# Optimization experiments

Hardware: AMD Instinct MI355X
Metric: run time of the kernel (lower is better)

## Reference

```python
import jax, jax.numpy as jnp
import numpy as np

ROPE_BASE = 100.0  # croco/dust3r RoPE2D default freq


def _rope1d(tok, pos1d, base=ROPE_BASE):
    # tok: [B,H,N,D], pos1d: [B,N] int
    D = tok.shape[-1]
    half = D // 2
    inv_freq = 1.0 / (base ** (jnp.arange(0, D, 2, dtype=jnp.float32) / D))  # [D/2]
    ang = pos1d[..., None].astype(jnp.float32) * inv_freq                    # [B,N,D/2]
    ang = jnp.concatenate([ang, ang], axis=-1)                               # [B,N,D]
    cos = jnp.cos(ang)[:, None, :, :].astype(tok.dtype)  # [B,1,N,D]
    sin = jnp.sin(ang)[:, None, :, :].astype(tok.dtype)
    t1, t2 = tok[..., :half], tok[..., half:]
    rot = jnp.concatenate([-t2, t1], axis=-1)  # rotate_half
    return tok * cos + rot * sin


def rope2d(tok, pos, base=ROPE_BASE):
    # tok: [B,H,N,C], pos: [B,N,2] (y,x) integer coords
    D = tok.shape[-1] // 2
    y = _rope1d(tok[..., :D], pos[..., 0], base)
    x = _rope1d(tok[..., D:], pos[..., 1], base)
    return jnp.concatenate([y, x], axis=-1)


def setup_inputs() -> dict:
    key = jax.random.key(0)
    k1, k2, k3, k4, k5 = jax.random.split(key, 5)
    B, H, N, C = 2, 12, 2049, 64
    q = jax.random.normal(k1, (B, H, N, C), dtype=jnp.float32)
    k = jax.random.normal(k2, (B, H, N, C), dtype=jnp.float32)
    v = jax.random.normal(k3, (B, H, N, C), dtype=jnp.float32)
    qpos = jax.random.randint(k4, (B, N, 2), 0, 64, dtype=jnp.int32)
    kpos = jax.random.randint(k5, (B, N, 2), 0, 64, dtype=jnp.int32)
    mask_for_attention = jnp.ones((B, N, N), dtype=bool)
    return {"q": q, "k": k, "v": v, "qpos": qpos, "kpos": kpos,
            "mask_for_attention": mask_for_attention, "num_cls": 1}


def reference(q, k, v, qpos, kpos, mask_for_attention, num_cls):
    B, H, Nq, C = q.shape
    scale = C ** -0.5
    # split off cls tokens, apply RoPE only to positional tokens
    q_nc = rope2d(q[:, :, num_cls:], qpos[:, num_cls:])
    k_nc = rope2d(k[:, :, num_cls:], kpos[:, num_cls:])
    # block similarity matrix:
    #            | K_cls |   K_pos    |
    #   | Q_cls |        sim_qcls_k   |
    #   |       | sim_q |-------------|
    #   | Q_pos |        |  sim_rope  |
    sim_rope = jnp.einsum('bhqc,bhkc->bhqk', q_nc, k_nc)                      # [B,H,Nq-cls,Nk-cls]
    sim_qcls_k = jnp.einsum('bhqc,bhkc->bhqk', q[:, :, :num_cls], k[:, :, num_cls:])
    sim_q = jnp.einsum('bhqc,bhkc->bhqk', q, k[:, :, :num_cls])               # [B,H,Nq,cls]
    sim = jnp.concatenate([sim_qcls_k, sim_rope], axis=-2)
    sim = jnp.concatenate([sim_q, sim], axis=-1)                              # [B,H,Nq,Nk]
    sim = sim * scale
    sim = jnp.where(mask_for_attention[:, None], sim, -jnp.inf)
    attn = jax.nn.softmax(sim, axis=-1)
    x = jnp.einsum('bhqk,bhkc->bhqc', attn, v)
    return x.transpose(0, 2, 1, 3).reshape(B, Nq, C * H)
```

## Files before the change

### kernel.cpp

```cpp
#include <hip/hip_runtime.h>
#include <hip/hip_bf16.h>

typedef __attribute__((ext_vector_type(8))) short bf16x8;
typedef __attribute__((ext_vector_type(4))) float f32x4;
typedef __attribute__((ext_vector_type(2))) float f32x2;
typedef unsigned short u16;

#define BN 2
#define HN 12
#define NN 2049
#define CN 64
#define NT 2048
#define BH 24
#define SCALE 0.125f
#define QSCL 0.1803368801111204f

__device__ __forceinline__ u16 f2bf(float x) {
  unsigned u = __builtin_bit_cast(unsigned, x);
  unsigned r = (u + 0x7fffu + ((u >> 16) & 1u)) >> 16;
  return (u16)r;
}

__device__ __forceinline__ unsigned cvt_pk(float lo, float hi) {
  unsigned r;
  asm("v_cvt_pk_bf16_f32 %0, %1, %2" : "=v"(r) : "v"(lo), "v"(hi));
  return r;
}

union PU {
  unsigned u[4];
  bf16x8 v;
};

__global__ __launch_bounds__(256) void rope_pack(
    const float* __restrict__ q, const float* __restrict__ k, const float* __restrict__ v,
    const int* __restrict__ qpos, const int* __restrict__ kpos,
    u16* __restrict__ Qr, u16* __restrict__ Kr, u16* __restrict__ Vt,
    float* __restrict__ S0, float* __restrict__ Pl, float* __restrict__ Po) {
  const int bh = blockIdx.x;
  const int t = blockIdx.y;
  const int b = bh / HN;
  const int tid = threadIdx.x;
  const int wv = tid >> 6, l = tid & 63;

  __shared__ float lutc[1024], luts[1024];
  __shared__ float qs[4096], ks[4096];
  __shared__ u16 ldsV[64][72];
  __shared__ float q0s[64], k0s[64];
  __shared__ float osum[4][64];
  __shared__ float psum[4];

  const int n0 = 1 + t * 64;
  const size_t base0 = (size_t)bh * NN * CN;

  const float LF = 6.6438561897747253f / 16.0f;
  for (int i = tid; i < 1024; i += 256) {
    const int pos = i >> 4, f = i & 15;
    const float inv = exp2f(-(float)f * LF);
    float sv, cv;
    sincosf((float)pos * inv, &sv, &cv);
    lutc[i] = cv;
    luts[i] = sv;
  }
  if (tid < 64) {
    q0s[tid] = q[base0 + tid];
    k0s[tid] = k[base0 + tid];
  }
  for (int e = tid; e < 4096; e += 256) {
    const int tok = e >> 6, c = e & 63;
    const size_t base = base0 + (size_t)(n0 + tok) * CN;
    qs[e] = q[base + c];
    ks[e] = k[base + c];
  }
  __syncthreads();

  float oacc = 0.f, pacc = 0.f;
  for (int i = 0; i < 16; ++i) {
    const int tok = i * 4 + wv;
    const int c = l;
    const int n = n0 + tok;
    const int cp = c & 31, f = cp & 15, axis = c >> 5;
    const int qp_ = qpos[((size_t)b * NN + n) * 2 + axis];
    const int kp_ = kpos[((size_t)b * NN + n) * 2 + axis];
    const float qa = qs[tok * 64 + c];
    const float ka = ks[tok * 64 + c];
    const float qrot = (cp < 16) ? -qs[tok * 64 + c + 16] : qs[tok * 64 + c - 16];
    const float krot = (cp < 16) ? -ks[tok * 64 + c + 16] : ks[tok * 64 + c - 16];
    Qr[((size_t)bh * NT + (n - 1)) * CN + c] =
        f2bf((qa * lutc[qp_ * 16 + f] + qrot * luts[qp_ * 16 + f]) * QSCL);
    Kr[((size_t)bh * NT + (n - 1)) * CN + c] =
        f2bf(ka * lutc[kp_ * 16 + f] + krot * luts[kp_ * 16 + f]);
    const float vv = v[base0 + (size_t)n * CN + c];
    ldsV[c][tok] = f2bf(vv);

    float pk = ka * q0s[c];
    float pq = qa * k0s[c];
    pk += __shfl_xor(pk, 1, 64);  pq += __shfl_xor(pq, 1, 64);
    pk += __shfl_xor(pk, 2, 64);  pq += __shfl_xor(pq, 2, 64);
    pk += __shfl_xor(pk, 4, 64);  pq += __shfl_xor(pq, 4, 64);
    pk += __shfl_xor(pk, 8, 64);  pq += __shfl_xor(pq, 8, 64);
    pk += __shfl_xor(pk, 16, 64); pq += __shfl_xor(pq, 16, 64);
    pk += __shfl_xor(pk, 32, 64); pq += __shfl_xor(pq, 32, 64);
    const float p = __builtin_amdgcn_exp2f(pk * QSCL);
    pacc += p;
    oacc += p * vv;
    if (l == 0) S0[(size_t)bh * NT + (n - 1)] = pq * QSCL;
  }
  osum[wv][l] = oacc;
  if (l == 0) psum[wv] = pacc;
  __syncthreads();

  for (int e = tid; e < 4096; e += 256) {
    const int c = e >> 6, tok = e & 63;
    Vt[((size_t)bh * CN + c) * NT + (t * 64 + tok)] = ldsV[c][tok];
  }
  if (tid < 64)
    Po[(size_t)(bh * 32 + t) * 64 + tid] =
        osum[0][tid] + osum[1][tid] + osum[2][tid] + osum[3][tid];
  if (tid == 0) Pl[bh * 32 + t] = psum[0] + psum[1] + psum[2] + psum[3];
}

__global__ __launch_bounds__(64) void row0_reduce(
    const float* __restrict__ q, const float* __restrict__ k, const float* __restrict__ v,
    const float* __restrict__ Pl, const float* __restrict__ Po, float* __restrict__ out) {
  const int bh = blockIdx.x;
  const int b = bh / HN, h = bh % HN;
  const int c = threadIdx.x;
  const size_t base0 = (size_t)bh * NN * CN;
  float pr = q[base0 + c] * k[base0 + c];
  pr += __shfl_xor(pr, 1, 64);
  pr += __shfl_xor(pr, 2, 64);
  pr += __shfl_xor(pr, 4, 64);
  pr += __shfl_xor(pr, 8, 64);
  pr += __shfl_xor(pr, 16, 64);
  pr += __shfl_xor(pr, 32, 64);
  const float p00 = __builtin_amdgcn_exp2f(pr * QSCL);
  float L = p00;
  float acc = p00 * v[base0 + c];
#pragma unroll
  for (int i = 0; i < 32; ++i) {
    L += Pl[bh * 32 + i];
    acc += Po[(size_t)(bh * 32 + i) * 64 + c];
  }
  out[(size_t)b * NN * (HN * CN) + h * CN + c] = acc / L;
}

__global__ __launch_bounds__(256) void attn_main(
    const float* __restrict__ v,
    const u16* __restrict__ Qr, const u16* __restrict__ Kr, const u16* __restrict__ Vt,
    const float* __restrict__ S0, float* __restrict__ out) {
  const int wg = blockIdx.x;
  const int bh = wg >> 5, qt = wg & 31;
  const int b = bh / HN, h = bh % HN;
  const int tid = threadIdx.x;
  const int wv = tid >> 6, l = tid & 63;
  const int l15 = l & 15, l4 = l >> 4;

  __shared__ u16 ldsK[2][4096];
  __shared__ u16 ldsV[2][4096];
  __shared__ float v0f[64];

  if (tid < 64) v0f[tid] = v[(size_t)bh * NN * CN + tid];
  __syncthreads();

  const int qrow = qt * 64 + wv * 16 + l15;
  const u16* qp = Qr + ((size_t)bh * NT + qrow) * CN;
  const bf16x8 qf0 = *reinterpret_cast<const bf16x8*>(qp + l4 * 8);
  const bf16x8 qf1 = *reinterpret_cast<const bf16x8*>(qp + 32 + l4 * 8);

  const float s0l2 = S0[(size_t)bh * NT + qrow];

  float lsum = (l4 == 0) ? __builtin_amdgcn_exp2f(s0l2) : 0.f;
  f32x4 o[4];
#pragma unroll
  for (int r = 0; r < 4; ++r) {
    const float p0 = __builtin_amdgcn_exp2f(__shfl(s0l2, (l4 << 2) | r, 64));
#pragma unroll
    for (int cf = 0; cf < 4; ++cf) o[cf][r] = p0 * v0f[cf * 16 + l15];
  }

  const u16* Kbh = Kr + (size_t)bh * NT * CN;
  const u16* Vbh = Vt + (size_t)bh * CN * NT;
  char* ldsKc = reinterpret_cast<char*>(&ldsK[0][0]);
  char* ldsVc = reinterpret_cast<char*>(&ldsV[0][0]);

  const int s16 = tid & 7, srowA = tid >> 3, srowB = (tid >> 3) + 32;
  const int swzA = (srowA & 7) << 4, swzB = (srowB & 7) << 4;
  const int kofsA = srowA * 128 + ((s16 * 16) ^ swzA);
  const int kofsB = srowB * 128 + ((s16 * 16) ^ swzB);
  const int pA = 2 * (32 * (s16 >> 2) + 8 * ((2 * s16) & 3) + 4 * ((s16 >> 1) & 1));
  const int pB = 2 * (32 * (s16 >> 2) + 8 * ((2 * s16 + 1) & 3) + 4 * ((s16 >> 1) & 1));
  const int vofsA0 = srowA * 128 + (pA ^ swzA);
  const int vofsA1 = srowA * 128 + (pB ^ swzA);
  const int vofsB0 = srowB * 128 + (pA ^ swzB);
  const int vofsB1 = srowB * 128 + (pB ^ swzB);

  f32x4 kreg[2], vrg[2];
#define LOAD_TILE(nx)                                                                       \
  do {                                                                                      \
    kreg[0] = *reinterpret_cast<const f32x4*>(Kbh + (size_t)((nx) + srowA) * CN + s16 * 8); \
    kreg[1] = *reinterpret_cast<const f32x4*>(Kbh + (size_t)((nx) + srowB) * CN + s16 * 8); \
    vrg[0] = *reinterpret_cast<const f32x4*>(Vbh + (size_t)srowA * NT + (nx) + s16 * 8);    \
    vrg[1] = *reinterpret_cast<const f32x4*>(Vbh + (size_t)srowB * NT + (nx) + s16 * 8);    \
  } while (0)

#define STAGE_WRITE(bofs)                                        \
  do {                                                           \
    *reinterpret_cast<f32x4*>(ldsKc + (bofs) + kofsA) = kreg[0]; \
    *reinterpret_cast<f32x4*>(ldsKc + (bofs) + kofsB) = kreg[1]; \
    f32x2 t0, t1, t2, t3;                                        \
    t0[0] = vrg[0][0]; t0[1] = vrg[0][1];                        \
    t1[0] = vrg[0][2]; t1[1] = vrg[0][3];                        \
    t2[0] = vrg[1][0]; t2[1] = vrg[1][1];                        \
    t3[0] = vrg[1][2]; t3[1] = vrg[1][3];                        \
    *reinterpret_cast<f32x2*>(ldsVc + (bofs) + vofsA0) = t0;     \
    *reinterpret_cast<f32x2*>(ldsVc + (bofs) + vofsA1) = t1;     \
    *reinterpret_cast<f32x2*>(ldsVc + (bofs) + vofsB0) = t2;     \
    *reinterpret_cast<f32x2*>(ldsVc + (bofs) + vofsB1) = t3;     \
  } while (0)

  LOAD_TILE(0);
  STAGE_WRITE(0);
  LOAD_TILE(64);

  for (int kt = 0; kt < 32; ++kt) {
    const int cur = (kt & 1) * 8192;
    const int nxt = ((kt + 1) & 1) * 8192;
    __syncthreads();
    if (kt < 31) {
      STAGE_WRITE(nxt);
      if (kt < 30) LOAD_TILE((kt + 2) * 64);
    }

    f32x4 S[4];
#pragma unroll
    for (int cf = 0; cf < 4; ++cf)
#pragma unroll
      for (int r = 0; r < 4; ++r) S[cf][r] = 0.f;
    __builtin_amdgcn_s_setprio(1);
#pragma unroll
    for (int kc = 0; kc < 2; ++kc) {
      const bf16x8 qf = (kc == 0) ? qf0 : qf1;
#pragma unroll
      for (int cf = 0; cf < 4; ++cf) {
        const int krow = cf * 16 + l15;
        const bf16x8 kb = *reinterpret_cast<const bf16x8*>(
            ldsKc + cur + krow * 128 + ((kc * 64 + l4 * 16) ^ ((krow & 7) << 4)));
        S[cf] = __builtin_amdgcn_mfma_f32_16x16x32_bf16(kb, qf, S[cf], 0, 0, 0);
      }
    }
    __builtin_amdgcn_s_setprio(0);

    unsigned W0[2], W1[2], W2[2], W3[2];
    {
      float e0, e1, e2, e3;
      e0 = __builtin_amdgcn_exp2f(S[0][0]); e1 = __builtin_amdgcn_exp2f(S[0][1]);
      e2 = __builtin_amdgcn_exp2f(S[0][2]); e3 = __builtin_amdgcn_exp2f(S[0][3]);
      lsum += (e0 + e1) + (e2 + e3);
      W0[0] = cvt_pk(e0, e1); W0[1] = cvt_pk(e2, e3);
      e0 = __builtin_amdgcn_exp2f(S[1][0]); e1 = __builtin_amdgcn_exp2f(S[1][1]);
      e2 = __builtin_amdgcn_exp2f(S[1][2]); e3 = __builtin_amdgcn_exp2f(S[1][3]);
      lsum += (e0 + e1) + (e2 + e3);
      W1[0] = cvt_pk(e0, e1); W1[1] = cvt_pk(e2, e3);
      e0 = __builtin_amdgcn_exp2f(S[2][0]); e1 = __builtin_amdgcn_exp2f(S[2][1]);
      e2 = __builtin_amdgcn_exp2f(S[2][2]); e3 = __builtin_amdgcn_exp2f(S[2][3]);
      lsum += (e0 + e1) + (e2 + e3);
      W2[0] = cvt_pk(e0, e1); W2[1] = cvt_pk(e2, e3);
      e0 = __builtin_amdgcn_exp2f(S[3][0]); e1 = __builtin_amdgcn_exp2f(S[3][1]);
      e2 = __builtin_amdgcn_exp2f(S[3][2]); e3 = __builtin_amdgcn_exp2f(S[3][3]);
      lsum += (e0 + e1) + (e2 + e3);
      W3[0] = cvt_pk(e0, e1); W3[1] = cvt_pk(e2, e3);
    }
    PU pu0, pu1;
    pu0.u[0] = W0[0]; pu0.u[1] = W0[1]; pu0.u[2] = W1[0]; pu0.u[3] = W1[1];
    pu1.u[0] = W2[0]; pu1.u[1] = W2[1]; pu1.u[2] = W3[0]; pu1.u[3] = W3[1];

    __builtin_amdgcn_s_setprio(1);
#pragma unroll
    for (int kc = 0; kc < 2; ++kc) {
      const bf16x8 pa = (kc == 0) ? pu0.v : pu1.v;
#pragma unroll
      for (int cf = 0; cf < 4; ++cf) {
        const int vrow = cf * 16 + l15;
        const bf16x8 vb = *reinterpret_cast<const bf16x8*>(
            ldsVc + cur + vrow * 128 + ((kc * 64 + l4 * 16) ^ ((vrow & 7) << 4)));
        o[cf] = __builtin_amdgcn_mfma_f32_16x16x32_bf16(pa, vb, o[cf], 0, 0, 0);
      }
    }
    __builtin_amdgcn_s_setprio(0);
  }

  float ls = lsum;
  ls += __shfl_xor(ls, 16, 64);
  ls += __shfl_xor(ls, 32, 64);
#pragma unroll
  for (int r = 0; r < 4; ++r) {
    const float invl = 1.0f / __shfl(ls, (l4 << 2) | r, 64);
    const int n = 1 + qt * 64 + wv * 16 + l4 * 4 + r;
    float* op = out + ((size_t)b * NN + n) * (HN * CN) + h * CN;
#pragma unroll
    for (int cf = 0; cf < 4; ++cf) op[cf * 16 + l15] = o[cf][r] * invl;
  }
#undef LOAD_TILE
#undef STAGE_WRITE
}

extern "C" void kernel_launch(void* const* d_in, const int* in_sizes, int n_in,
                              void* d_out, int out_size, void* d_ws, size_t ws_size,
                              hipStream_t stream) {
  const float* q = (const float*)d_in[0];
  const float* k = (const float*)d_in[1];
  const float* v = (const float*)d_in[2];
  const int* qpos = (const int*)d_in[3];
  const int* kpos = (const int*)d_in[4];
  float* out = (float*)d_out;

  u16* Qr = (u16*)d_ws;
  u16* Kr = Qr + (size_t)BH * NT * CN;
  u16* Vt = Kr + (size_t)BH * NT * CN;
  float* S0 = (float*)(Vt + (size_t)BH * NT * CN);
  float* Pl = S0 + (size_t)BH * NT;
  float* Po = Pl + BH * 32;

  rope_pack<<<dim3(BH, 32), 256, 0, stream>>>(q, k, v, qpos, kpos, Qr, Kr, Vt, S0, Pl, Po);
  row0_reduce<<<dim3(BH), 64, 0, stream>>>(q, k, v, Pl, Po, out);
  attn_main<<<dim3(BH * 32), 256, 0, stream>>>(v, Qr, Kr, Vt, S0, out);
}
```

Before: 65.93 us.

## Switch attention main loop to 32x32x16 MFMA with 128-row query tiles

Replaces the 16x16x32 bf16 MFMA tiling with 32x32x16 MFMAs, so each wave now handles 32 query rows and each workgroup 128. This halves the K/V LDS traffic per query and reduces instruction count per FLOP. The V staging layout, softmax packing and output store are adapted to the new fragment layout, and output stores become vectorized float4. The grid is halved to 384 blocks with a remapped bh/qt index, which lowers parallelism and raises register pressure from the larger accumulators.

```diff
diff --git a/kernel.cpp b/kernel.cpp
--- a/kernel.cpp
+++ b/kernel.cpp
@@ -2,6 +2,7 @@
 #include <hip/hip_bf16.h>
 
 typedef __attribute__((ext_vector_type(8))) short bf16x8;
+typedef __attribute__((ext_vector_type(16))) float f32x16;
 typedef __attribute__((ext_vector_type(4))) float f32x4;
 typedef __attribute__((ext_vector_type(2))) float f32x2;
 typedef unsigned short u16;
@@ -12,7 +13,6 @@
 #define CN 64
 #define NT 2048
 #define BH 24
-#define SCALE 0.125f
 #define QSCL 0.1803368801111204f
 
 __device__ __forceinline__ u16 f2bf(float x) {
@@ -150,34 +150,35 @@
     const u16* __restrict__ Qr, const u16* __restrict__ Kr, const u16* __restrict__ Vt,
     const float* __restrict__ S0, float* __restrict__ out) {
   const int wg = blockIdx.x;
-  const int bh = wg >> 5, qt = wg & 31;
+  const int bh = 3 * (wg & 7) + ((wg >> 3) >> 4);
+  const int qt = (wg >> 3) & 15;
   const int b = bh / HN, h = bh % HN;
   const int tid = threadIdx.x;
   const int wv = tid >> 6, l = tid & 63;
-  const int l15 = l & 15, l4 = l >> 4;
+  const int l31 = l & 31, lh = l >> 5;
 
   __shared__ u16 ldsK[2][4096];
   __shared__ u16 ldsV[2][4096];
   __shared__ float v0f[64];
-
   if (tid < 64) v0f[tid] = v[(size_t)bh * NN * CN + tid];
   __syncthreads();
 
-  const int qrow = qt * 64 + wv * 16 + l15;
-  const u16* qp = Qr + ((size_t)bh * NT + qrow) * CN;
-  const bf16x8 qf0 = *reinterpret_cast<const bf16x8*>(qp + l4 * 8);
-  const bf16x8 qf1 = *reinterpret_cast<const bf16x8*>(qp + 32 + l4 * 8);
+  const int qrow = qt * 128 + wv * 32 + l31;
+  const u16* qp = Qr + ((size_t)bh * NT + qrow) * CN + lh * 8;
+  bf16x8 qf[4];
+#pragma unroll
+  for (int s = 0; s < 4; ++s) qf[s] = *reinterpret_cast<const bf16x8*>(qp + s * 16);
 
   const float s0l2 = S0[(size_t)bh * NT + qrow];
-
-  float lsum = (l4 == 0) ? __builtin_amdgcn_exp2f(s0l2) : 0.f;
-  f32x4 o[4];
-#pragma unroll
-  for (int r = 0; r < 4; ++r) {
-    const float p0 = __builtin_amdgcn_exp2f(__shfl(s0l2, (l4 << 2) | r, 64));
-#pragma unroll
-    for (int cf = 0; cf < 4; ++cf) o[cf][r] = p0 * v0f[cf * 16 + l15];
-  }
+  const float p0 = __builtin_amdgcn_exp2f(s0l2);
+  float lsum = (lh == 0) ? p0 : 0.f;
+
+  f32x16 o[2];
+#pragma unroll
+  for (int half = 0; half < 2; ++half)
+#pragma unroll
+    for (int reg = 0; reg < 16; ++reg)
+      o[half][reg] = p0 * v0f[(reg & 3) + 8 * (reg >> 2) + 4 * lh + 32 * half];
 
   const u16* Kbh = Kr + (size_t)bh * NT * CN;
   const u16* Vbh = Vt + (size_t)bh * CN * NT;
@@ -188,12 +189,12 @@
   const int swzA = (srowA & 7) << 4, swzB = (srowB & 7) << 4;
   const int kofsA = srowA * 128 + ((s16 * 16) ^ swzA);
   const int kofsB = srowB * 128 + ((s16 * 16) ^ swzB);
-  const int pA = 2 * (32 * (s16 >> 2) + 8 * ((2 * s16) & 3) + 4 * ((s16 >> 1) & 1));
-  const int pB = 2 * (32 * (s16 >> 2) + 8 * ((2 * s16 + 1) & 3) + 4 * ((s16 >> 1) & 1));
-  const int vofsA0 = srowA * 128 + (pA ^ swzA);
-  const int vofsA1 = srowA * 128 + (pB ^ swzA);
-  const int vofsB0 = srowB * 128 + (pA ^ swzB);
-  const int vofsB1 = srowB * 128 + (pB ^ swzB);
+  const int vb1 = 32 * (s16 >> 1) + 8 * (s16 & 1);
+  const int vb2 = vb1 + 16;
+  const int vofsA0 = srowA * 128 + (vb1 ^ swzA);
+  const int vofsA1 = srowA * 128 + (vb2 ^ swzA);
+  const int vofsB0 = srowB * 128 + (vb1 ^ swzB);
+  const int vofsB1 = srowB * 128 + (vb2 ^ swzB);
 
   f32x4 kreg[2], vrg[2];
 #define LOAD_TILE(nx)                                                                       \
@@ -223,6 +224,7 @@
   STAGE_WRITE(0);
   LOAD_TILE(64);
 
+#pragma unroll 2
   for (int kt = 0; kt < 32; ++kt) {
     const int cur = (kt & 1) * 8192;
     const int nxt = ((kt + 1) & 1) * 8192;
@@ -232,74 +234,71 @@
       if (kt < 30) LOAD_TILE((kt + 2) * 64);
     }
 
-    f32x4 S[4];
-#pragma unroll
-    for (int cf = 0; cf < 4; ++cf)
-#pragma unroll
-      for (int r = 0; r < 4; ++r) S[cf][r] = 0.f;
+    f32x16 S[2];
+#pragma unroll
+    for (int th = 0; th < 2; ++th)
+#pragma unroll
+      for (int reg = 0; reg < 16; ++reg) S[th][reg] = 0.f;
     __builtin_amdgcn_s_setprio(1);
 #pragma unroll
-    for (int kc = 0; kc < 2; ++kc) {
-      const bf16x8 qf = (kc == 0) ? qf0 : qf1;
-#pragma unroll
-      for (int cf = 0; cf < 4; ++cf) {
-        const int krow = cf * 16 + l15;
+    for (int th = 0; th < 2; ++th) {
+      const int trow = th * 32 + l31;
+      const int tswz = (trow & 7) << 4;
+#pragma unroll
+      for (int st = 0; st < 4; ++st) {
         const bf16x8 kb = *reinterpret_cast<const bf16x8*>(
-            ldsKc + cur + krow * 128 + ((kc * 64 + l4 * 16) ^ ((krow & 7) << 4)));
-        S[cf] = __builtin_amdgcn_mfma_f32_16x16x32_bf16(kb, qf, S[cf], 0, 0, 0);
+            ldsKc + cur + trow * 128 + ((st * 32 + lh * 16) ^ tswz));
+        S[th] = __builtin_amdgcn_mfma_f32_32x32x16_bf16(kb, qf[st], S[th], 0, 0, 0);
       }
     }
     __builtin_amdgcn_s_setprio(0);
 
-    unsigned W0[2], W1[2], W2[2], W3[2];
-    {
-      float e0, e1, e2, e3;
-      e0 = __builtin_amdgcn_exp2f(S[0][0]); e1 = __builtin_amdgcn_exp2f(S[0][1]);
-      e2 = __builtin_amdgcn_exp2f(S[0][2]); e3 = __builtin_amdgcn_exp2f(S[0][3]);
-      lsum += (e0 + e1) + (e2 + e3);
-      W0[0] = cvt_pk(e0, e1); W0[1] = cvt_pk(e2, e3);
-      e0 = __builtin_amdgcn_exp2f(S[1][0]); e1 = __builtin_amdgcn_exp2f(S[1][1]);
-      e2 = __builtin_amdgcn_exp2f(S[1][2]); e3 = __builtin_amdgcn_exp2f(S[1][3]);
-      lsum += (e0 + e1) + (e2 + e3);
-      W1[0] = cvt_pk(e0, e1); W1[1] = cvt_pk(e2, e3);
-      e0 = __builtin_amdgcn_exp2f(S[2][0]); e1 = __builtin_amdgcn_exp2f(S[2][1]);
-      e2 = __builtin_amdgcn_exp2f(S[2][2]); e3 = __builtin_amdgcn_exp2f(S[2][3]);
-      lsum += (e0 + e1) + (e2 + e3);
-      W2[0] = cvt_pk(e0, e1); W2[1] = cvt_pk(e2, e3);
-      e0 = __builtin_amdgcn_exp2f(S[3][0]); e1 = __builtin_amdgcn_exp2f(S[3][1]);
-      e2 = __builtin_amdgcn_exp2f(S[3][2]); e3 = __builtin_amdgcn_exp2f(S[3][3]);
-      lsum += (e0 + e1) + (e2 + e3);
-      W3[0] = cvt_pk(e0, e1); W3[1] = cvt_pk(e2, e3);
-    }
-    PU pu0, pu1;
-    pu0.u[0] = W0[0]; pu0.u[1] = W0[1]; pu0.u[2] = W1[0]; pu0.u[3] = W1[1];
-    pu1.u[0] = W2[0]; pu1.u[1] = W2[1]; pu1.u[2] = W3[0]; pu1.u[3] = W3[1];
+    PU pa[4];
+#pragma unroll
+    for (int th = 0; th < 2; ++th) {
+      float e[16];
+#pragma unroll
+      for (int reg = 0; reg < 16; ++reg) e[reg] = __builtin_amdgcn_exp2f(S[th][reg]);
+#pragma unroll
+      for (int reg = 0; reg < 16; reg += 4)
+        lsum += (e[reg] + e[reg + 1]) + (e[reg + 2] + e[reg + 3]);
+#pragma unroll
+      for (int sp = 0; sp < 2; ++sp) {
+#pragma unroll
+        for (int m = 0; m < 4; ++m)
+          pa[2 * th + sp].u[m] = cvt_pk(e[8 * sp + 2 * m], e[8 * sp + 2 * m + 1]);
+      }
+    }
 
     __builtin_amdgcn_s_setprio(1);
 #pragma unroll
-    for (int kc = 0; kc < 2; ++kc) {
-      const bf16x8 pa = (kc == 0) ? pu0.v : pu1.v;
-#pragma unroll
-      for (int cf = 0; cf < 4; ++cf) {
-        const int vrow = cf * 16 + l15;
+    for (int half = 0; half < 2; ++half) {
+      const int crow = half * 32 + l31;
+      const int cswz = (crow & 7) << 4;
+#pragma unroll
+      for (int s = 0; s < 4; ++s) {
         const bf16x8 vb = *reinterpret_cast<const bf16x8*>(
-            ldsVc + cur + vrow * 128 + ((kc * 64 + l4 * 16) ^ ((vrow & 7) << 4)));
-        o[cf] = __builtin_amdgcn_mfma_f32_16x16x32_bf16(pa, vb, o[cf], 0, 0, 0);
+            ldsVc + cur + crow * 128 + ((s * 32 + lh * 16) ^ cswz));
+        o[half] = __builtin_amdgcn_mfma_f32_32x32x16_bf16(vb, pa[s].v, o[half], 0, 0, 0);
       }
     }
     __builtin_amdgcn_s_setprio(0);
   }
 
   float ls = lsum;
-  ls += __shfl_xor(ls, 16, 64);
   ls += __shfl_xor(ls, 32, 64);
-#pragma unroll
-  for (int r = 0; r < 4; ++r) {
-    const float invl = 1.0f / __shfl(ls, (l4 << 2) | r, 64);
-    const int n = 1 + qt * 64 + wv * 16 + l4 * 4 + r;
-    float* op = out + ((size_t)b * NN + n) * (HN * CN) + h * CN;
-#pragma unroll
-    for (int cf = 0; cf < 4; ++cf) op[cf * 16 + l15] = o[cf][r] * invl;
+  const float invl = 1.0f / ls;
+  const int n = 1 + qrow;
+  float* op = out + ((size_t)b * NN + n) * (HN * CN) + h * CN;
+#pragma unroll
+  for (int half = 0; half < 2; ++half) {
+#pragma unroll
+    for (int rq = 0; rq < 4; ++rq) {
+      f32x4 val;
+#pragma unroll
+      for (int j = 0; j < 4; ++j) val[j] = o[half][4 * rq + j] * invl;
+      *reinterpret_cast<f32x4*>(op + 8 * rq + 4 * lh + 32 * half) = val;
+    }
   }
 #undef LOAD_TILE
 #undef STAGE_WRITE
@@ -324,5 +323,5 @@
 
   rope_pack<<<dim3(BH, 32), 256, 0, stream>>>(q, k, v, qpos, kpos, Qr, Kr, Vt, S0, Pl, Po);
   row0_reduce<<<dim3(BH), 64, 0, stream>>>(q, k, v, Pl, Po, out);
-  attn_main<<<dim3(BH * 32), 256, 0, stream>>>(v, Qr, Kr, Vt, S0, out);
-}
+  attn_main<<<dim3(BH * 16), 256, 0, stream>>>(v, Qr, Kr, Vt, S0, out);
+}
```

Result: slower. 68.99 us (+4.6%).
